# Performance work log

Hardware: AMD Instinct MI355X
Metric: run time of the kernel (lower is better)

Reference implementation:

```python
import jax, jax.numpy as jnp
import numpy as np

N = 500000      # nodes
E = 1250000     # edges
S = 50000       # subgraphs
G = 64          # graphs
D = 64          # hidden dim (M_in = M_out = 64)
NLAYERS = 5


def setup_inputs() -> dict:
    key = jax.random.key(0)
    ks = jax.random.split(key, 24)

    def p(k, shape):
        return jax.random.normal(k, shape, dtype=jnp.float32) * 0.05

    return {
        "z": jax.random.randint(ks[0], (N,), 0, 100),
        "edge_index": jax.random.randint(ks[1], (2, E), 0, N),
        "node_to_subgraph": jax.random.randint(ks[2], (N,), 0, S),
        "subgraph_to_graph": jax.random.randint(ks[3], (S,), 0, G),
        # per-layer params (stacked over the 5 conv layers)
        "z_tables": p(ks[4], (NLAYERS, 100, D)),      # Embedding(100, 64) x5
        "tf_W": p(ks[5], (NLAYERS - 1, D, 2 * D)),    # Linear(128, 64) for layers 1..4
        "tf_b": p(ks[6], (NLAYERS - 1, D)),
        "ggc_W": p(ks[7], (NLAYERS, D, D)),           # GatedGraphConv weight[0]
        "gru_wih": p(ks[8], (NLAYERS, 3 * D, D)),
        "gru_whh": p(ks[9], (NLAYERS, 3 * D, D)),
        "gru_bih": p(ks[10], (NLAYERS, 3 * D)),
        "gru_bhh": p(ks[11], (NLAYERS, 3 * D)),
        # head
        "fc1_W": p(ks[12], (32, D)), "fc1_b": p(ks[13], (32,)),
        "fc2_W": p(ks[14], (16, 32)), "fc2_b": p(ks[15], (16,)),
        "fc3_W": p(ks[16], (1, 16)), "fc3_b": p(ks[17], (1,)),
    }


def reference(z, edge_index, node_to_subgraph, subgraph_to_graph,
              z_tables, tf_W, tf_b, ggc_W,
              gru_wih, gru_whh, gru_bih, gru_bhh,
              fc1_W, fc1_b, fc2_W, fc2_b, fc3_W, fc3_b):
    src, dst = edge_index[0], edge_index[1]
    x = None
    for layer in range(NLAYERS):
        ze = z_tables[layer][z]                      # [N, 64] embedding lookup
        if x is None:
            x = ze
        else:
            x = jnp.concatenate([x, ze], axis=-1) @ tf_W[layer - 1].T + tf_b[layer - 1]
        # GatedGraphConv with num_layers=1: m = x @ W; add-aggregate; GRUCell update
        m = x @ ggc_W[layer]                          # [N, 64]
        agg = jax.ops.segment_sum(m[src], dst, num_segments=N)  # scatter-add to dst
        gi = agg @ gru_wih[layer].T + gru_bih[layer]  # [N, 192]
        gh = x @ gru_whh[layer].T + gru_bhh[layer]    # [N, 192]
        ir, iz, inn = jnp.split(gi, 3, axis=-1)
        hr, hz, hn = jnp.split(gh, 3, axis=-1)
        r = jax.nn.sigmoid(ir + hr)
        u = jax.nn.sigmoid(iz + hz)
        n = jnp.tanh(inn + r * hn)
        x = (1.0 - u) * n + u * x
    # subgraph pooling ('mean' branch actually does global_add_pool)
    x = jax.ops.segment_sum(x, node_to_subgraph, num_segments=S)   # [S, 64]
    # graph pooling (y_ndim == 1)
    x = jax.ops.segment_sum(x, subgraph_to_graph, num_segments=G)  # [G, 64]
    x = jax.nn.elu(x @ fc1_W.T + fc1_b)
    x = jax.nn.elu(x @ fc2_W.T + fc2_b)
    return x @ fc3_W.T + fc3_b                        # [G, 1]
```

## Files before the change

kernel.cpp:

```cpp
#include <hip/hip_runtime.h>
#include <hip/hip_bf16.h>

#define NN 500000
#define EE 1250000
#define NP 501760
#define NBLK 489
#define GCAP 16384

typedef __attribute__((ext_vector_type(8))) short bf16x8;
typedef __attribute__((ext_vector_type(4))) float f32x4;

__device__ __forceinline__ float ngnn97_bf2f(unsigned short u) {
  return __uint_as_float(((unsigned int)u) << 16);
}
__device__ __forceinline__ unsigned short ngnn97_f2bf(float f) {
  union { __hip_bfloat16 b; unsigned short u; } cv;
  cv.b = __float2bfloat16(f);
  return cv.u;
}

__global__ void ngnn97_code(float* __restrict__ out, float v) {
  if (threadIdx.x < 64) out[threadIdx.x] = v;
}

__global__ __launch_bounds__(256) void ngnn97_pre(
    const float* __restrict__ ggc, const float* __restrict__ wih,
    const float* __restrict__ whh, const float* __restrict__ bih,
    const float* __restrict__ bhh, const float* __restrict__ tfW,
    const float* __restrict__ ztab,
    unsigned short* __restrict__ Ubt, float* __restrict__ Ub,
    unsigned short* __restrict__ Vbt, unsigned short* __restrict__ ztabh) {
  int idx = blockIdx.x * 256 + threadIdx.x;
  if (idx < 163840) {
    int l = idx >> 15, r = idx & 32767;
    int n = r >> 7, k = r & 127;
    float v = 0.f;
    if (k < 64) {
      if (n < 192) {
        const float* gp = ggc + l * 4096 + k * 64;
        const float* wp = wih + l * 12288 + n * 64;
        float acc = 0.f;
#pragma unroll
        for (int t2 = 0; t2 < 64; t2++) acc = fmaf(gp[t2], wp[t2], acc);
        v = acc;
      }
    } else {
      int k2 = k - 64;
      if (n < 128) v = whh[l * 12288 + n * 64 + k2];
      else if (n >= 192) v = whh[l * 12288 + (n - 64) * 64 + k2];
    }
    Ubt[idx] = ngnn97_f2bf(v);
  } else if (idx < 196608) {
    int i2 = idx - 163840;
    Vbt[i2] = ngnn97_f2bf(tfW[i2]);
  } else if (idx < 197888) {
    int i2 = idx - 196608;
    int l = i2 >> 8, j = i2 & 255;
    float v;
    if (j < 128)      v = bih[l * 192 + j] + bhh[l * 192 + j];
    else if (j < 192) v = bih[l * 192 + j];
    else              v = bhh[l * 192 + j - 64];
    Ub[i2] = v;
  } else if (idx < 229888) {
    int i2 = idx - 197888;
    ztabh[i2] = ngnn97_f2bf(ztab[i2]);
  }
}

__global__ __launch_bounds__(256) void ngnn97_hist(const int* __restrict__ dst, int* __restrict__ counts) {
  int e = blockIdx.x * 256 + threadIdx.x;
  if (e < EE) atomicAdd(&counts[dst[e]], 1);
}

__global__ __launch_bounds__(256) void ngnn97_red(const int* __restrict__ counts, int* __restrict__ bsum) {
  __shared__ int s[256];
  int t = threadIdx.x, base = blockIdx.x * 1024;
  int v = 0;
#pragma unroll
  for (int i = 0; i < 4; i++) v += counts[base + t + i * 256];
  s[t] = v; __syncthreads();
  for (int o = 128; o > 0; o >>= 1) { if (t < o) s[t] += s[t + o]; __syncthreads(); }
  if (t == 0) bsum[blockIdx.x] = s[0];
}

__global__ __launch_bounds__(512) void ngnn97_scan1(const int* __restrict__ bsum, int* __restrict__ boff) {
  __shared__ int s[512];
  int t = threadIdx.x;
  int v = (t < NBLK) ? bsum[t] : 0;
  s[t] = v; __syncthreads();
  for (int o = 1; o < 512; o <<= 1) {
    int a = (t >= o) ? s[t - o] : 0;
    __syncthreads(); s[t] += a; __syncthreads();
  }
  if (t < NBLK) boff[t] = s[t] - v;
}

__global__ __launch_bounds__(256) void ngnn97_scan2(const int* __restrict__ counts, const int* __restrict__ boff,
                                                    int* __restrict__ row_ptr, int* __restrict__ cursor) {
  __shared__ int s[256];
  int t = threadIdx.x, base = blockIdx.x * 1024;
  int4 c = *(const int4*)(counts + base + t * 4);
  int tsum = c.x + c.y + c.z + c.w;
  s[t] = tsum; __syncthreads();
  for (int o = 1; o < 256; o <<= 1) {
    int a = (t >= o) ? s[t - o] : 0;
    __syncthreads(); s[t] += a; __syncthreads();
  }
  int off = boff[blockIdx.x] + s[t] - tsum;
  int4 r;
  r.x = off; r.y = off + c.x; r.z = off + c.x + c.y; r.w = off + c.x + c.y + c.z;
  *(int4*)(row_ptr + base + t * 4) = r;
  *(int4*)(cursor + base + t * 4) = r;
}

__global__ __launch_bounds__(256) void ngnn97_fill(const int* __restrict__ src, const int* __restrict__ dst,
                                                   int* __restrict__ cursor, int* __restrict__ srcs) {
  int e = blockIdx.x * 256 + threadIdx.x;
  if (e < EE) {
    int pos = atomicAdd(&cursor[dst[e]], 1);
    srcs[pos] = src[e];
  }
}

__global__ __launch_bounds__(256) void ngnn97_g8(const int* __restrict__ n2s, const int* __restrict__ s2g,
                                                 unsigned char* __restrict__ g8) {
  int idx = blockIdx.x * 256 + threadIdx.x;
  if (idx < NN) g8[idx] = (unsigned char)s2g[n2s[idx]];
}

__global__ __launch_bounds__(256) void ngnn97_bucket(const unsigned char* __restrict__ g8,
                                                     int* __restrict__ gcur, int* __restrict__ nlist) {
  __shared__ int hcnt[64];
  __shared__ int hbase[64];
  int t = threadIdx.x;
  int base = blockIdx.x * 1024;
  if (t < 64) hcnt[t] = 0;
  __syncthreads();
#pragma unroll
  for (int i = 0; i < 4; i++) {
    int node = base + i * 256 + t;
    if (node < NN) atomicAdd(&hcnt[g8[node]], 1);
  }
  __syncthreads();
  if (t < 64) {
    int c = hcnt[t];
    hbase[t] = (c > 0) ? atomicAdd(&gcur[t], c) : 0;
    hcnt[t] = 0;
  }
  __syncthreads();
#pragma unroll
  for (int i = 0; i < 4; i++) {
    int node = base + i * 256 + t;
    if (node < NN) {
      int g = g8[node];
      int loc = atomicAdd(&hcnt[g], 1);
      int pos = hbase[g] + loc;
      if (pos < GCAP) nlist[g * GCAP + pos] = node;
    }
  }
}

__global__ __launch_bounds__(256) void ngnn97_embed(const int* __restrict__ z,
                                                    const unsigned short* __restrict__ ztabh,
                                                    unsigned short* __restrict__ xh) {
  int idx = blockIdx.x * 256 + threadIdx.x;
  int node = idx >> 3, sub = idx & 7;
  if (node < NN) {
    int zz = z[node];
    *(bf16x8*)(xh + (size_t)node * 64 + sub * 8) =
        *(const bf16x8*)(ztabh + zz * 64 + sub * 8);
  }
}

__global__ __launch_bounds__(256) void ngnn97_agg(const unsigned short* __restrict__ xh,
                                                  const int* __restrict__ rowp,
                                                  const int* __restrict__ srcs,
                                                  unsigned short* __restrict__ aggx) {
  int t = threadIdx.x;
  int wv = t >> 6, lane = t & 63;
  int grp = lane >> 3, sub = lane & 7;
  int node = blockIdx.x * 32 + wv * 8 + grp;
  if (node >= NN) return;
  int b = rowp[node], e = rowp[node + 1];
  float acc[8];
#pragma unroll
  for (int i = 0; i < 8; i++) acc[i] = 0.f;
  int p = b;
  for (; p + 2 <= e; p += 2) {
    int s0 = srcs[p], s1 = srcs[p + 1];
    bf16x8 v0 = *(const bf16x8*)(xh + (size_t)s0 * 64 + sub * 8);
    bf16x8 v1 = *(const bf16x8*)(xh + (size_t)s1 * 64 + sub * 8);
#pragma unroll
    for (int i = 0; i < 8; i++)
      acc[i] += ngnn97_bf2f((unsigned short)v0[i]) + ngnn97_bf2f((unsigned short)v1[i]);
  }
  if (p < e) {
    int s0 = srcs[p];
    bf16x8 v0 = *(const bf16x8*)(xh + (size_t)s0 * 64 + sub * 8);
#pragma unroll
    for (int i = 0; i < 8; i++) acc[i] += ngnn97_bf2f((unsigned short)v0[i]);
  }
  bf16x8 ov;
#pragma unroll
  for (int i = 0; i < 8; i++) ov[i] = (short)ngnn97_f2bf(acc[i]);
  *(bf16x8*)(aggx + (size_t)node * 64 + sub * 8) = ov;
}

__global__ __launch_bounds__(256, 4) void ngnn97_gru(
    unsigned short* __restrict__ xh, const unsigned short* __restrict__ aggx,
    const unsigned short* __restrict__ Ubt, const float* __restrict__ Ub,
    const unsigned short* __restrict__ Vbt, const float* __restrict__ tfb,
    const int* __restrict__ z, const unsigned short* __restrict__ ztabh,
    int do_transform) {
  __shared__ unsigned short Abuf[128 * 72];
  const int t = threadIdx.x;
  const int lane = t & 63, w = t >> 6;
  const int ncol = lane & 15, quad = lane >> 4;
  const int nbase = blockIdx.x * 128;
  const int strip = 32 * w;

#pragma unroll
  for (int i = 0; i < 8; i++) {
    int chunk = i * 64 + lane;
    int r2 = chunk >> 4, c4 = (chunk & 15) << 2;
    int node = nbase + strip + r2;
    ushort4 qx = make_ushort4(0, 0, 0, 0);
    if (node < NN) qx = *(const ushort4*)(xh + (size_t)node * 64 + c4);
    *(ushort4*)(Abuf + (strip + r2) * 72 + c4) = qx;
  }

  bf16x8 afrA[2][2], afrX[2][2];
#pragma unroll
  for (int mm = 0; mm < 2; mm++) {
    int node = nbase + strip + mm * 16 + ncol;
#pragma unroll
    for (int kc = 0; kc < 2; kc++) {
      bf16x8 va = (bf16x8){0, 0, 0, 0, 0, 0, 0, 0};
      if (node < NN) va = *(const bf16x8*)(aggx + (size_t)node * 64 + quad * 8 + kc * 32);
      afrA[mm][kc] = va;
      afrX[mm][kc] = *(const bf16x8*)(Abuf + (strip + mm * 16 + ncol) * 72 + quad * 8 + kc * 32);
    }
  }

#pragma unroll
  for (int c = 0; c < 4; c++) {
    f32x4 aR[2], aZ[2], aN[2], aH[2];
#pragma unroll
    for (int mm = 0; mm < 2; mm++) {
      aR[mm] = (f32x4){0.f, 0.f, 0.f, 0.f}; aZ[mm] = aR[mm];
      aN[mm] = aR[mm]; aH[mm] = aR[mm];
    }
#pragma unroll
    for (int kc = 0; kc < 4; kc++) {
      const unsigned short* ub = Ubt + (size_t)(c * 16 + ncol) * 128 + quad * 8 + kc * 32;
      bf16x8 bR = *(const bf16x8*)(ub);
      bf16x8 bZ = *(const bf16x8*)(ub + 64 * 128);
      bf16x8 bX = (kc < 2) ? *(const bf16x8*)(ub + 128 * 128)
                           : *(const bf16x8*)(ub + 192 * 128);
#pragma unroll
      for (int mm = 0; mm < 2; mm++) {
        bf16x8 a = (kc < 2) ? afrA[mm][kc] : afrX[mm][kc - 2];
        aR[mm] = __builtin_amdgcn_mfma_f32_16x16x32_bf16(a, bR, aR[mm], 0, 0, 0);
        aZ[mm] = __builtin_amdgcn_mfma_f32_16x16x32_bf16(a, bZ, aZ[mm], 0, 0, 0);
        if (kc < 2) aN[mm] = __builtin_amdgcn_mfma_f32_16x16x32_bf16(a, bX, aN[mm], 0, 0, 0);
        else        aH[mm] = __builtin_amdgcn_mfma_f32_16x16x32_bf16(a, bX, aH[mm], 0, 0, 0);
      }
    }
    int j = c * 16 + ncol;
    float bRs = Ub[j], bZs = Ub[64 + j], bNs = Ub[128 + j], bHs = Ub[192 + j];
#pragma unroll
    for (int mm = 0; mm < 2; mm++)
#pragma unroll
      for (int r = 0; r < 4; r++) {
        int row = strip + mm * 16 + quad * 4 + r;
        float R = aR[mm][r] + bRs, Z = aZ[mm][r] + bZs;
        float Nv = aN[mm][r] + bNs, H = aH[mm][r] + bHs;
        float rg = 1.f / (1.f + __expf(-R));
        float ug = 1.f / (1.f + __expf(-Z));
        float e2 = __expf(2.f * (Nv + rg * H));
        float nn2 = 1.f - 2.f / (e2 + 1.f);
        float xo = ngnn97_bf2f(Abuf[row * 72 + j]);
        Abuf[row * 72 + j] = ngnn97_f2bf((1.f - ug) * nn2 + ug * xo);
      }
  }

  if (do_transform) {
    bf16x8 afrN[2][2], afrE[2][2];
#pragma unroll
    for (int mm = 0; mm < 2; mm++) {
      int node = nbase + strip + mm * 16 + ncol;
      int zz = (node < NN) ? z[node] : 0;
#pragma unroll
      for (int kc = 0; kc < 2; kc++) {
        afrN[mm][kc] = *(const bf16x8*)(Abuf + (strip + mm * 16 + ncol) * 72 + quad * 8 + kc * 32);
        afrE[mm][kc] = *(const bf16x8*)(ztabh + zz * 64 + quad * 8 + kc * 32);
      }
    }
#pragma unroll
    for (int c2 = 0; c2 < 4; c2++) {
      f32x4 acc[2];
      acc[0] = (f32x4){0.f, 0.f, 0.f, 0.f}; acc[1] = acc[0];
#pragma unroll
      for (int kc = 0; kc < 4; kc++) {
        bf16x8 bV = *(const bf16x8*)(Vbt + (size_t)(c2 * 16 + ncol) * 128 + quad * 8 + kc * 32);
#pragma unroll
        for (int mm = 0; mm < 2; mm++) {
          bf16x8 a = (kc < 2) ? afrN[mm][kc] : afrE[mm][kc - 2];
          acc[mm] = __builtin_amdgcn_mfma_f32_16x16x32_bf16(a, bV, acc[mm], 0, 0, 0);
        }
      }
      int j = c2 * 16 + ncol;
      float bt = tfb[j];
#pragma unroll
      for (int mm = 0; mm < 2; mm++)
#pragma unroll
        for (int r = 0; r < 4; r++) {
          int row = strip + mm * 16 + quad * 4 + r;
          Abuf[row * 72 + j] = ngnn97_f2bf(acc[mm][r] + bt);
        }
    }
  }

#pragma unroll
  for (int i = 0; i < 8; i++) {
    int chunk = i * 64 + lane;
    int r2 = chunk >> 4, c4 = (chunk & 15) << 2;
    int node = nbase + strip + r2;
    if (node < NN)
      *(ushort4*)(xh + (size_t)node * 64 + c4) = *(const ushort4*)(Abuf + (strip + r2) * 72 + c4);
  }
}

__global__ __launch_bounds__(256) void ngnn97_pool(const unsigned short* __restrict__ xh,
                                                   const int* __restrict__ nlist,
                                                   const int* __restrict__ gcur,
                                                   float* __restrict__ gpool) {
  __shared__ float part[4][64];
  int t = threadIdx.x;
  int lane = t & 63, wv = t >> 6;
  int g = blockIdx.x >> 4, c = blockIdx.x & 15;
  int cnt = gcur[g];
  if (cnt > GCAP) cnt = GCAP;
  int r0 = (c * cnt) >> 4, r1 = ((c + 1) * cnt) >> 4;
  const int* nl = nlist + g * GCAP;
  float a0 = 0.f, a1 = 0.f;
  int r = r0 + wv;
  for (; r + 4 < r1; r += 8) {
    int n0 = nl[r], n1 = nl[r + 4];
    a0 += ngnn97_bf2f(xh[(size_t)n0 * 64 + lane]);
    a1 += ngnn97_bf2f(xh[(size_t)n1 * 64 + lane]);
  }
  if (r < r1) a0 += ngnn97_bf2f(xh[(size_t)nl[r] * 64 + lane]);
  part[wv][lane] = a0 + a1;
  __syncthreads();
  if (t < 64)
    atomicAdd(&gpool[g * 64 + t], part[0][t] + part[1][t] + part[2][t] + part[3][t]);
}

__global__ __launch_bounds__(256) void ngnn97_head(
    const float* __restrict__ gpool,
    const float* __restrict__ W1, const float* __restrict__ b1,
    const float* __restrict__ W2, const float* __restrict__ b2,
    const float* __restrict__ W3, const float* __restrict__ b3,
    float* __restrict__ out) {
  __shared__ float gp[4096];
  __shared__ float h1[2048];
  __shared__ float h2[1024];
  int t = threadIdx.x;
  for (int i = t; i < 4096; i += 256) gp[i] = gpool[i];
  __syncthreads();
  for (int i = t; i < 2048; i += 256) {
    int g = i >> 5, o = i & 31;
    float a = b1[o];
    for (int d = 0; d < 64; d++) a = fmaf(gp[g * 64 + d], W1[o * 64 + d], a);
    h1[i] = (a > 0.f) ? a : (__expf(a) - 1.f);
  }
  __syncthreads();
  for (int i = t; i < 1024; i += 256) {
    int g = i >> 4, o = i & 15;
    float a = b2[o];
    for (int d = 0; d < 32; d++) a = fmaf(h1[g * 32 + d], W2[o * 32 + d], a);
    h2[i] = (a > 0.f) ? a : (__expf(a) - 1.f);
  }
  __syncthreads();
  if (t < 64) {
    float a = b3[0];
    for (int d = 0; d < 16; d++) a = fmaf(h2[t * 16 + d], W3[d], a);
    out[t] = a;
  }
}

#define OFF_XH    ((size_t)0)
#define OFF_AGG   ((size_t)64000000)
#define OFF_CNT   ((size_t)128000000)
#define OFF_ROW   (OFF_CNT + (size_t)NP * 4)
#define OFF_CUR   (OFF_ROW + (size_t)NP * 4)
#define OFF_SRC   (OFF_CUR + (size_t)NP * 4)
#define OFF_BSUM  (OFF_SRC + (size_t)EE * 4)
#define OFF_BOFF  (OFF_BSUM + (size_t)2048)
#define OFF_U     (OFF_BOFF + (size_t)2048)
#define OFF_UB    (OFF_U + (size_t)327680)
#define OFF_V     (OFF_UB + (size_t)5120)
#define OFF_GP    (OFF_V + (size_t)65536)
#define OFF_G8    (OFF_GP + (size_t)16384)
#define OFF_ZTH   (OFF_G8 + (size_t)500736)
#define OFF_GCUR  (OFF_ZTH + (size_t)64000)
#define OFF_NL    (OFF_GCUR + (size_t)1024)
#define WS_NEED   (OFF_NL + (size_t)64 * GCAP * 4)

extern "C" void kernel_launch(void* const* d_in, const int* in_sizes, int n_in,
                              void* d_out, int out_size, void* d_ws, size_t ws_size,
                              hipStream_t stream) {
  float* out = (float*)d_out;
  if (ws_size < WS_NEED) {
    ngnn97_code<<<1, 64, 0, stream>>>(out, 7.0f);
    return;
  }

  const int* z    = (const int*)d_in[0];
  const int* ei   = (const int*)d_in[1];
  const int* n2s  = (const int*)d_in[2];
  const int* s2g  = (const int*)d_in[3];
  const float* ztab = (const float*)d_in[4];
  const float* tfW  = (const float*)d_in[5];
  const float* tfb  = (const float*)d_in[6];
  const float* ggc  = (const float*)d_in[7];
  const float* wih  = (const float*)d_in[8];
  const float* whh  = (const float*)d_in[9];
  const float* bih  = (const float*)d_in[10];
  const float* bhh  = (const float*)d_in[11];
  const float* W1   = (const float*)d_in[12];
  const float* b1   = (const float*)d_in[13];
  const float* W2   = (const float*)d_in[14];
  const float* b2   = (const float*)d_in[15];
  const float* W3   = (const float*)d_in[16];
  const float* b3   = (const float*)d_in[17];

  char* ws = (char*)d_ws;
  unsigned short* xh     = (unsigned short*)(ws + OFF_XH);
  unsigned short* aggx   = (unsigned short*)(ws + OFF_AGG);
  int*            counts = (int*)(ws + OFF_CNT);
  int*            rowp   = (int*)(ws + OFF_ROW);
  int*            curs   = (int*)(ws + OFF_CUR);
  int*            srcs   = (int*)(ws + OFF_SRC);
  int*            bsum   = (int*)(ws + OFF_BSUM);
  int*            boff   = (int*)(ws + OFF_BOFF);
  unsigned short* Ubt    = (unsigned short*)(ws + OFF_U);
  float*          Ub     = (float*)(ws + OFF_UB);
  unsigned short* Vbt    = (unsigned short*)(ws + OFF_V);
  float*          gpool  = (float*)(ws + OFF_GP);
  unsigned char*  g8     = (unsigned char*)(ws + OFF_G8);
  unsigned short* ztabh  = (unsigned short*)(ws + OFF_ZTH);
  int*            gcur   = (int*)(ws + OFF_GCUR);
  int*            nlist  = (int*)(ws + OFF_NL);

  hipMemsetAsync(counts, 0, (size_t)NP * 4, stream);
  hipMemsetAsync(gpool, 0, 16384, stream);
  hipMemsetAsync(gcur, 0, 1024, stream);

  ngnn97_pre<<<899, 256, 0, stream>>>(ggc, wih, whh, bih, bhh, tfW, ztab, Ubt, Ub, Vbt, ztabh);
  ngnn97_g8<<<(NN + 255) / 256, 256, 0, stream>>>(n2s, s2g, g8);
  ngnn97_bucket<<<NBLK, 256, 0, stream>>>(g8, gcur, nlist);

  const int* srcp = ei;
  const int* dstp = ei + EE;
  ngnn97_hist<<<(EE + 255) / 256, 256, 0, stream>>>(dstp, counts);
  ngnn97_red<<<NBLK, 256, 0, stream>>>(counts, bsum);
  ngnn97_scan1<<<1, 512, 0, stream>>>(bsum, boff);
  ngnn97_scan2<<<NBLK, 256, 0, stream>>>(counts, boff, rowp, curs);
  ngnn97_fill<<<(EE + 255) / 256, 256, 0, stream>>>(srcp, dstp, curs, srcs);

  ngnn97_embed<<<(NN * 8 + 255) / 256, 256, 0, stream>>>(z, ztabh, xh);

  for (int l = 0; l < 5; l++) {
    ngnn97_agg<<<(NN + 31) / 32, 256, 0, stream>>>(xh, rowp, srcs, aggx);
    ngnn97_gru<<<(NN + 127) / 128, 256, 0, stream>>>(
        xh, aggx, Ubt + (size_t)l * 32768, Ub + (size_t)l * 256,
        Vbt + (size_t)(l < 4 ? l : 0) * 8192, tfb + (size_t)(l < 4 ? l : 0) * 64,
        z, ztabh + (size_t)(l < 4 ? l + 1 : 0) * 6400, (l < 4) ? 1 : 0);
  }

  ngnn97_pool<<<1024, 256, 0, stream>>>(xh, nlist, gcur, gpool);
  ngnn97_head<<<1, 256, 0, stream>>>(gpool, W1, b1, W2, b2, W3, b3, out);
}
```

Measured before the change: 1.225 ms.

## Fuse neighbor aggregation into GRU kernel with ping-pong node feature buffers

Removes the separate aggregation kernel and computes each block's 128-node neighbor sums directly into shared memory inside the GRU kernel. This avoids writing and re-reading the aggregate buffer and one launch per layer. Node features now alternate between two buffers, so gathering from old features cannot race with writes of new ones. The risk is that the gather's irregular, latency-bound work now runs inside a register-heavy MFMA kernel, which may hide latency less well. A redundant dead shared-memory read was also added.

```diff
diff --git a/kernel.cpp b/kernel.cpp
--- a/kernel.cpp
+++ b/kernel.cpp
@@ -172,42 +172,9 @@
   }
 }
 
-__global__ __launch_bounds__(256) void ngnn97_agg(const unsigned short* __restrict__ xh,
-                                                  const int* __restrict__ rowp,
-                                                  const int* __restrict__ srcs,
-                                                  unsigned short* __restrict__ aggx) {
-  int t = threadIdx.x;
-  int wv = t >> 6, lane = t & 63;
-  int grp = lane >> 3, sub = lane & 7;
-  int node = blockIdx.x * 32 + wv * 8 + grp;
-  if (node >= NN) return;
-  int b = rowp[node], e = rowp[node + 1];
-  float acc[8];
-#pragma unroll
-  for (int i = 0; i < 8; i++) acc[i] = 0.f;
-  int p = b;
-  for (; p + 2 <= e; p += 2) {
-    int s0 = srcs[p], s1 = srcs[p + 1];
-    bf16x8 v0 = *(const bf16x8*)(xh + (size_t)s0 * 64 + sub * 8);
-    bf16x8 v1 = *(const bf16x8*)(xh + (size_t)s1 * 64 + sub * 8);
-#pragma unroll
-    for (int i = 0; i < 8; i++)
-      acc[i] += ngnn97_bf2f((unsigned short)v0[i]) + ngnn97_bf2f((unsigned short)v1[i]);
-  }
-  if (p < e) {
-    int s0 = srcs[p];
-    bf16x8 v0 = *(const bf16x8*)(xh + (size_t)s0 * 64 + sub * 8);
-#pragma unroll
-    for (int i = 0; i < 8; i++) acc[i] += ngnn97_bf2f((unsigned short)v0[i]);
-  }
-  bf16x8 ov;
-#pragma unroll
-  for (int i = 0; i < 8; i++) ov[i] = (short)ngnn97_f2bf(acc[i]);
-  *(bf16x8*)(aggx + (size_t)node * 64 + sub * 8) = ov;
-}
-
 __global__ __launch_bounds__(256, 4) void ngnn97_gru(
-    unsigned short* __restrict__ xh, const unsigned short* __restrict__ aggx,
+    const unsigned short* __restrict__ xh_old, unsigned short* __restrict__ xh_new,
+    const int* __restrict__ rowp, const int* __restrict__ srcs,
     const unsigned short* __restrict__ Ubt, const float* __restrict__ Ub,
     const unsigned short* __restrict__ Vbt, const float* __restrict__ tfb,
     const int* __restrict__ z, const unsigned short* __restrict__ ztabh,
@@ -219,28 +186,62 @@
   const int nbase = blockIdx.x * 128;
   const int strip = 32 * w;
 
+  {
+    int grp = lane >> 3, sub = lane & 7;
+#pragma unroll
+    for (int sb = 0; sb < 4; sb++) {
+      int row = strip + sb * 8 + grp;
+      int node = nbase + row;
+      float acc[8];
+#pragma unroll
+      for (int i = 0; i < 8; i++) acc[i] = 0.f;
+      if (node < NN) {
+        int b = rowp[node], e = rowp[node + 1];
+        int p = b;
+        for (; p + 2 <= e; p += 2) {
+          int s0 = srcs[p], s1 = srcs[p + 1];
+          bf16x8 v0 = *(const bf16x8*)(xh_old + (size_t)s0 * 64 + sub * 8);
+          bf16x8 v1 = *(const bf16x8*)(xh_old + (size_t)s1 * 64 + sub * 8);
+#pragma unroll
+          for (int i = 0; i < 8; i++)
+            acc[i] += ngnn97_bf2f((unsigned short)v0[i]) + ngnn97_bf2f((unsigned short)v1[i]);
+        }
+        if (p < e) {
+          bf16x8 v0 = *(const bf16x8*)(xh_old + (size_t)srcs[p] * 64 + sub * 8);
+#pragma unroll
+          for (int i = 0; i < 8; i++) acc[i] += ngnn97_bf2f((unsigned short)v0[i]);
+        }
+      }
+      bf16x8 ov;
+#pragma unroll
+      for (int i = 0; i < 8; i++) ov[i] = (short)ngnn97_f2bf(acc[i]);
+      *(bf16x8*)(Abuf + row * 72 + sub * 8) = ov;
+    }
+  }
+
+  bf16x8 afrA[2][2];
+#pragma unroll
+  for (int mm = 0; mm < 2; mm++)
+#pragma unroll
+    for (int kc = 0; kc < 2; kc++)
+      afrA[mm][kc] = *(const bf16x8*)(Abuf + (strip + mm * 16 + ncol) * 72 + quad * 8 + kc * 32);
+
 #pragma unroll
   for (int i = 0; i < 8; i++) {
     int chunk = i * 64 + lane;
     int r2 = chunk >> 4, c4 = (chunk & 15) << 2;
     int node = nbase + strip + r2;
     ushort4 qx = make_ushort4(0, 0, 0, 0);
-    if (node < NN) qx = *(const ushort4*)(xh + (size_t)node * 64 + c4);
+    if (node < NN) qx = *(const ushort4*)(xh_old + (size_t)node * 64 + c4);
     *(ushort4*)(Abuf + (strip + r2) * 72 + c4) = qx;
   }
 
-  bf16x8 afrA[2][2], afrX[2][2];
-#pragma unroll
-  for (int mm = 0; mm < 2; mm++) {
-    int node = nbase + strip + mm * 16 + ncol;
-#pragma unroll
-    for (int kc = 0; kc < 2; kc++) {
-      bf16x8 va = (bf16x8){0, 0, 0, 0, 0, 0, 0, 0};
-      if (node < NN) va = *(const bf16x8*)(aggx + (size_t)node * 64 + quad * 8 + kc * 32);
-      afrA[mm][kc] = va;
+  bf16x8 afrX[2][2];
+#pragma unroll
+  for (int mm = 0; mm < 2; mm++)
+#pragma unroll
+    for (int kc = 0; kc < 2; kc++)
       afrX[mm][kc] = *(const bf16x8*)(Abuf + (strip + mm * 16 + ncol) * 72 + quad * 8 + kc * 32);
-    }
-  }
 
 #pragma unroll
   for (int c = 0; c < 4; c++) {
@@ -279,7 +280,8 @@
         float ug = 1.f / (1.f + __expf(-Z));
         float e2 = __expf(2.f * (Nv + rg * H));
         float nn2 = 1.f - 2.f / (e2 + 1.f);
-        float xo = ngnn97_bf2f(Abuf[row * 72 + j]);
+        float xo = ngnn97_bf2f(Abuf[row * 72 + 64 + j - c * 16 + c * 16]);
+        xo = ngnn97_bf2f(Abuf[row * 72 + j]);
         Abuf[row * 72 + j] = ngnn97_f2bf((1.f - ug) * nn2 + ug * xo);
       }
   }
@@ -327,7 +329,7 @@
     int r2 = chunk >> 4, c4 = (chunk & 15) << 2;
     int node = nbase + strip + r2;
     if (node < NN)
-      *(ushort4*)(xh + (size_t)node * 64 + c4) = *(const ushort4*)(Abuf + (strip + r2) * 72 + c4);
+      *(ushort4*)(xh_new + (size_t)node * 64 + c4) = *(const ushort4*)(Abuf + (strip + r2) * 72 + c4);
   }
 }
 
@@ -390,8 +392,8 @@
   }
 }
 
-#define OFF_XH    ((size_t)0)
-#define OFF_AGG   ((size_t)64000000)
+#define OFF_XH0   ((size_t)0)
+#define OFF_XH1   ((size_t)64000000)
 #define OFF_CNT   ((size_t)128000000)
 #define OFF_ROW   (OFF_CNT + (size_t)NP * 4)
 #define OFF_CUR   (OFF_ROW + (size_t)NP * 4)
@@ -437,8 +439,8 @@
   const float* b3   = (const float*)d_in[17];
 
   char* ws = (char*)d_ws;
-  unsigned short* xh     = (unsigned short*)(ws + OFF_XH);
-  unsigned short* aggx   = (unsigned short*)(ws + OFF_AGG);
+  unsigned short* xh0    = (unsigned short*)(ws + OFF_XH0);
+  unsigned short* xh1    = (unsigned short*)(ws + OFF_XH1);
   int*            counts = (int*)(ws + OFF_CNT);
   int*            rowp   = (int*)(ws + OFF_ROW);
   int*            curs   = (int*)(ws + OFF_CUR);
@@ -470,16 +472,19 @@
   ngnn97_scan2<<<NBLK, 256, 0, stream>>>(counts, boff, rowp, curs);
   ngnn97_fill<<<(EE + 255) / 256, 256, 0, stream>>>(srcp, dstp, curs, srcs);
 
-  ngnn97_embed<<<(NN * 8 + 255) / 256, 256, 0, stream>>>(z, ztabh, xh);
-
+  ngnn97_embed<<<(NN * 8 + 255) / 256, 256, 0, stream>>>(z, ztabh, xh0);
+
+  unsigned short* xc = xh0;
+  unsigned short* xn2 = xh1;
   for (int l = 0; l < 5; l++) {
-    ngnn97_agg<<<(NN + 31) / 32, 256, 0, stream>>>(xh, rowp, srcs, aggx);
     ngnn97_gru<<<(NN + 127) / 128, 256, 0, stream>>>(
-        xh, aggx, Ubt + (size_t)l * 32768, Ub + (size_t)l * 256,
+        xc, xn2, rowp, srcs,
+        Ubt + (size_t)l * 32768, Ub + (size_t)l * 256,
         Vbt + (size_t)(l < 4 ? l : 0) * 8192, tfb + (size_t)(l < 4 ? l : 0) * 64,
         z, ztabh + (size_t)(l < 4 ? l + 1 : 0) * 6400, (l < 4) ? 1 : 0);
-  }
-
-  ngnn97_pool<<<1024, 256, 0, stream>>>(xh, nlist, gcur, gpool);
+    unsigned short* tmp = xc; xc = xn2; xn2 = tmp;
+  }
+
+  ngnn97_pool<<<1024, 256, 0, stream>>>(xc, nlist, gcur, gpool);
   ngnn97_head<<<1, 256, 0, stream>>>(gpool, W1, b1, W2, b2, W3, b3, out);
 }
```

Result: faster. 1.164 ms (-5.0%).
